# Kernel tuning notes

Hardware: AMD Instinct MI355X
Metric: run time of the kernel (lower is better)

The kernel has to match this reference:

```python
import jax, jax.numpy as jnp
import numpy as np

B, L1, L2, DIM_HID = 32, 64, 64, 256
FEAT = 2 * DIM_HID  # per-sequence feature dim; pair dim = 4*dim_hid


def setup_inputs() -> dict:
    key = jax.random.key(0)
    k1, k2, k3, k4, k5, k6 = jax.random.split(key, 6)
    x1 = jax.random.normal(k1, (B, L1, FEAT), dtype=jnp.float32)
    x2 = jax.random.normal(k2, (B, L2, FEAT), dtype=jnp.float32)
    # lengths in [1, L]; force max length so torch's dynamic max_len == L1*L2
    seq_lens1 = jax.random.randint(k3, (B,), 1, L1 + 1).at[0].set(L1)
    seq_lens2 = jax.random.randint(k4, (B,), 1, L2 + 1).at[0].set(L2)
    W = jax.random.normal(k5, (DIM_HID, 4 * DIM_HID), dtype=jnp.float32) * (1.0 / np.sqrt(4 * DIM_HID))
    b = jax.random.normal(k6, (DIM_HID,), dtype=jnp.float32) * 0.01
    return {"x1": x1, "seq_lens1": seq_lens1, "x2": x2, "seq_lens2": seq_lens2, "W": W, "b": b}


def reference(x1, seq_lens1, x2, seq_lens2, W, b):
    # Faithful to torch: for each sample, all (i,j) pairs with i<sl1, j<sl2 get
    # feature concat(x1[i], x2[j]); remaining rows (up to max_len = L1*L2) are
    # zero-padded BEFORE Linear+ReLU, so they contribute relu(b) to the sum.
    # Linear on concat == split GEMM: x1 @ W[:, :F].T + x2 @ W[:, F:].T + b,
    # which avoids materializing the [B, L1*L2, 4h] pair tensor.
    y1 = jnp.einsum('bif,hf->bih', x1, W[:, :FEAT])  # [B, L1, H]
    y2 = jnp.einsum('bjf,hf->bjh', x2, W[:, FEAT:])  # [B, L2, H]
    mask = (jnp.arange(L1)[None, :] < seq_lens1[:, None])[:, :, None] & \
           (jnp.arange(L2)[None, :] < seq_lens2[:, None])[:, None, :]  # [B, L1, L2]
    z = jnp.where(mask[..., None], y1[:, :, None, :] + y2[:, None, :, :] + b, b)
    y = jax.nn.relu(z)  # [B, L1, L2, H]; dropout is identity (eval / p handled)
    denom = (seq_lens1 * seq_lens2).astype(x1.dtype)[:, None]
    return y.sum(axis=(1, 2)) / denom
```

## Files before the change

kernel.cpp:

```cpp
#include <hip/hip_runtime.h>

#define BB 32
#define LL 64
#define HH 256
#define FF 512
#define WSTRIDE 1024
#define HT 16
#define BK 64
#define NKT (FF / BK)
#define YSTR 17

#define A1OFF 0
#define A2OFF 16384
#define W1OFF 32768
#define W2OFF 36864
#define BUFB  40960

typedef float float4v __attribute__((ext_vector_type(4)));
typedef short short8  __attribute__((ext_vector_type(8)));

static __device__ __forceinline__ unsigned int cvt_pk_bf16(float lo, float hi) {
    unsigned int r;
    asm("v_cvt_pk_bf16_f32 %0, %1, %2" : "=v"(r) : "v"(lo), "v"(hi));
    return r;
}

static __device__ __forceinline__ short8 cvt8(float4 lo, float4 hi) {
    union { short8 s; unsigned int u[4]; } o;
    o.u[0] = cvt_pk_bf16(lo.x, lo.y);
    o.u[1] = cvt_pk_bf16(lo.z, lo.w);
    o.u[2] = cvt_pk_bf16(hi.x, hi.y);
    o.u[3] = cvt_pk_bf16(hi.z, hi.w);
    return o.s;
}

static __device__ __forceinline__ void gl16(const float* g, void* l) {
    __builtin_amdgcn_global_load_lds(
        (const __attribute__((address_space(1))) void*)(const void*)g,
        (__attribute__((address_space(3))) void*)l, 16, 0, 0);
}

__global__ __launch_bounds__(256)
void fused_kernel(const float* __restrict__ x1,
                  const float* __restrict__ x2,
                  const float* __restrict__ W,
                  const int* __restrict__ s1p,
                  const int* __restrict__ s2p,
                  const float* __restrict__ bias,
                  float* __restrict__ out) {
    const int b  = blockIdx.x;
    const int h0 = blockIdx.y * HT;

    __shared__ __align__(16) unsigned char smem[2 * BUFB];
    float (*y1t)[YSTR]     = (float (*)[YSTR])(smem);
    float (*y2t)[YSTR]     = (float (*)[YSTR])(smem + 4352);
    float (*partial)[YSTR] = (float (*)[YSTR])(smem + 8704);

    const int t      = threadIdx.x;
    const int lane   = t & 63;
    const int wid    = t >> 6;
    const int srcSel = wid >> 1;
    const int mrow   = (wid & 1) * 32;
    const int lm     = lane & 15;
    const int quad   = lane >> 4;

    const int srow = t >> 4;
    const int sg   = (t & 15) ^ (srow & 7);

    const float* a1g = x1 + (size_t)(b * LL + srow) * FF + sg * 4;
    const float* a2g = x2 + (size_t)(b * LL + srow) * FF + sg * 4;
    const float* w1g = W + (size_t)(h0 + srow) * WSTRIDE + sg * 4;
    const float* w2g = w1g + FF;

    float4v acc[2];
    acc[0] = (float4v){0.f, 0.f, 0.f, 0.f};
    acc[1] = (float4v){0.f, 0.f, 0.f, 0.f};

    const int m     = lm & 7;
    const int offLo = (((quad * 2)     ^ m) * 16);
    const int offHi = (((quad * 2 + 1) ^ m) * 16);
    const int aRowOff = (srcSel ? A2OFF : A1OFF) + (mrow + lm) * 256;
    const int bRowOff = (srcSel ? W2OFF : W1OFF) + lm * 256;

    auto issue = [&](int kt, int bsel) {
        unsigned char* Lb = smem + bsel * BUFB;
        const int ko = kt * BK;
        #pragma unroll
        for (int q = 0; q < 4; ++q) {
            gl16(a1g + ko + (size_t)q * (16 * FF), Lb + A1OFF + q * 4096 + wid * 1024);
            gl16(a2g + ko + (size_t)q * (16 * FF), Lb + A2OFF + q * 4096 + wid * 1024);
        }
        gl16(w1g + ko, Lb + W1OFF + wid * 1024);
        gl16(w2g + ko, Lb + W2OFF + wid * 1024);
    };

    issue(0, 0);
    __syncthreads();

    for (int kt = 0; kt < NKT; ++kt) {
        if (kt + 1 < NKT) issue(kt + 1, (kt + 1) & 1);

        const unsigned char* Lb  = smem + (kt & 1) * BUFB;
        const unsigned char* pA0 = Lb + aRowOff;
        const unsigned char* pA1 = pA0 + 16 * 256;
        const unsigned char* pB  = Lb + bRowOff;

        #pragma unroll
        for (int ks = 0; ks < 2; ++ks) {
            const int kb = ks * 128;
            const float4 a0lo = *(const float4*)(pA0 + kb + offLo);
            const float4 a0hi = *(const float4*)(pA0 + kb + offHi);
            const float4 a1lo = *(const float4*)(pA1 + kb + offLo);
            const float4 a1hi = *(const float4*)(pA1 + kb + offHi);
            const float4 blo  = *(const float4*)(pB  + kb + offLo);
            const float4 bhi  = *(const float4*)(pB  + kb + offHi);
            const short8 a0 = cvt8(a0lo, a0hi);
            const short8 a1 = cvt8(a1lo, a1hi);
            const short8 b0 = cvt8(blo, bhi);
            acc[0] = __builtin_amdgcn_mfma_f32_16x16x32_bf16(a0, b0, acc[0], 0, 0, 0);
            acc[1] = __builtin_amdgcn_mfma_f32_16x16x32_bf16(a1, b0, acc[1], 0, 0, 0);
        }
        __syncthreads();
    }

    {
        float (*yt)[YSTR] = srcSel ? y2t : y1t;
        const float bv = srcSel ? bias[h0 + lm] : 0.0f;
        #pragma unroll
        for (int im = 0; im < 2; ++im)
            #pragma unroll
            for (int j = 0; j < 4; ++j)
                yt[mrow + im * 16 + quad * 4 + j][lm] = acc[im][j] + bv;
    }
    __syncthreads();

    const int n1 = s1p[b];
    const int n2 = s2p[b];
    const int h  = t & 15;
    const int ic = t >> 4;

    float r1[4];
    #pragma unroll
    for (int ii = 0; ii < 4; ++ii) {
        const int i = ic * 4 + ii;
        r1[ii] = (i < n1) ? y1t[i][h] : -1e30f;
    }

    float ac[4] = {0.f, 0.f, 0.f, 0.f};
    int j = 0;
    for (; j + 4 <= n2; j += 4) {
        const float v0 = y2t[j][h];
        const float v1 = y2t[j + 1][h];
        const float v2 = y2t[j + 2][h];
        const float v3 = y2t[j + 3][h];
        #pragma unroll
        for (int ii = 0; ii < 4; ++ii) {
            ac[ii] += fmaxf(r1[ii] + v0, 0.f);
            ac[ii] += fmaxf(r1[ii] + v1, 0.f);
            ac[ii] += fmaxf(r1[ii] + v2, 0.f);
            ac[ii] += fmaxf(r1[ii] + v3, 0.f);
        }
    }
    for (; j < n2; ++j) {
        const float v0 = y2t[j][h];
        #pragma unroll
        for (int ii = 0; ii < 4; ++ii)
            ac[ii] += fmaxf(r1[ii] + v0, 0.f);
    }
    partial[ic][h] = (ac[0] + ac[1]) + (ac[2] + ac[3]);
    __syncthreads();

    if (t < HT) {
        float s = 0.f;
        #pragma unroll
        for (int ic2 = 0; ic2 < 16; ++ic2)
            s += partial[ic2][t];
        const float denom = (float)(n1 * n2);
        const float pad = (float)(LL * LL) - denom;
        out[b * HH + h0 + t] = (s + pad * fmaxf(bias[h0 + t], 0.f)) / denom;
    }
}

extern "C" void kernel_launch(void* const* d_in, const int* in_sizes, int n_in,
                              void* d_out, int out_size, void* d_ws, size_t ws_size,
                              hipStream_t stream) {
    const float* x1 = (const float*)d_in[0];
    const int*   s1 = (const int*)d_in[1];
    const float* x2 = (const float*)d_in[2];
    const int*   s2 = (const int*)d_in[3];
    const float* W  = (const float*)d_in[4];
    const float* b  = (const float*)d_in[5];
    float* out = (float*)d_out;
    (void)d_ws; (void)ws_size;

    fused_kernel<<<dim3(BB, HH / HT), 256, 0, stream>>>(x1, x2, W, s1, s2, b, out);
}
```

Measured before the change: 76.93 us.

## Load GEMM operands directly from global into registers, dropping LDS staging

Replaces the double-buffered global-to-LDS async staging pipeline with direct per-lane float4 global loads feeding the bf16 MFMA. LDS use drops to the small reduction tables, which removes the per-tile barriers and could raise occupancy. In exchange, global loads are no longer coalesced across the wave's rows, and the latency overlap now relies on loop unrolling rather than explicit prefetch.

```diff
diff --git a/kernel.cpp b/kernel.cpp
--- a/kernel.cpp
+++ b/kernel.cpp
@@ -6,15 +6,7 @@
 #define FF 512
 #define WSTRIDE 1024
 #define HT 16
-#define BK 64
-#define NKT (FF / BK)
 #define YSTR 17
-
-#define A1OFF 0
-#define A2OFF 16384
-#define W1OFF 32768
-#define W2OFF 36864
-#define BUFB  40960
 
 typedef float float4v __attribute__((ext_vector_type(4)));
 typedef short short8  __attribute__((ext_vector_type(8)));
@@ -34,12 +26,6 @@
     return o.s;
 }
 
-static __device__ __forceinline__ void gl16(const float* g, void* l) {
-    __builtin_amdgcn_global_load_lds(
-        (const __attribute__((address_space(1))) void*)(const void*)g,
-        (__attribute__((address_space(3))) void*)l, 16, 0, 0);
-}
-
 __global__ __launch_bounds__(256)
 void fused_kernel(const float* __restrict__ x1,
                   const float* __restrict__ x2,
@@ -51,10 +37,9 @@
     const int b  = blockIdx.x;
     const int h0 = blockIdx.y * HT;
 
-    __shared__ __align__(16) unsigned char smem[2 * BUFB];
-    float (*y1t)[YSTR]     = (float (*)[YSTR])(smem);
-    float (*y2t)[YSTR]     = (float (*)[YSTR])(smem + 4352);
-    float (*partial)[YSTR] = (float (*)[YSTR])(smem + 8704);
+    __shared__ float y1t[LL][YSTR];
+    __shared__ float y2t[LL][YSTR];
+    __shared__ float partial[16][YSTR];
 
     const int t      = threadIdx.x;
     const int lane   = t & 63;
@@ -64,63 +49,29 @@
     const int lm     = lane & 15;
     const int quad   = lane >> 4;
 
-    const int srow = t >> 4;
-    const int sg   = (t & 15) ^ (srow & 7);
-
-    const float* a1g = x1 + (size_t)(b * LL + srow) * FF + sg * 4;
-    const float* a2g = x2 + (size_t)(b * LL + srow) * FF + sg * 4;
-    const float* w1g = W + (size_t)(h0 + srow) * WSTRIDE + sg * 4;
-    const float* w2g = w1g + FF;
+    const float* Xsrc = srcSel ? x2 : x1;
+    const float* aRow0 = Xsrc + (size_t)(b * LL + mrow + lm) * FF + quad * 8;
+    const float* aRow1 = aRow0 + (size_t)16 * FF;
+    const float* bRow  = W + (size_t)(h0 + lm) * WSTRIDE + srcSel * FF + quad * 8;
 
     float4v acc[2];
     acc[0] = (float4v){0.f, 0.f, 0.f, 0.f};
     acc[1] = (float4v){0.f, 0.f, 0.f, 0.f};
 
-    const int m     = lm & 7;
-    const int offLo = (((quad * 2)     ^ m) * 16);
-    const int offHi = (((quad * 2 + 1) ^ m) * 16);
-    const int aRowOff = (srcSel ? A2OFF : A1OFF) + (mrow + lm) * 256;
-    const int bRowOff = (srcSel ? W2OFF : W1OFF) + lm * 256;
-
-    auto issue = [&](int kt, int bsel) {
-        unsigned char* Lb = smem + bsel * BUFB;
-        const int ko = kt * BK;
-        #pragma unroll
-        for (int q = 0; q < 4; ++q) {
-            gl16(a1g + ko + (size_t)q * (16 * FF), Lb + A1OFF + q * 4096 + wid * 1024);
-            gl16(a2g + ko + (size_t)q * (16 * FF), Lb + A2OFF + q * 4096 + wid * 1024);
-        }
-        gl16(w1g + ko, Lb + W1OFF + wid * 1024);
-        gl16(w2g + ko, Lb + W2OFF + wid * 1024);
-    };
-
-    issue(0, 0);
-    __syncthreads();
-
-    for (int kt = 0; kt < NKT; ++kt) {
-        if (kt + 1 < NKT) issue(kt + 1, (kt + 1) & 1);
-
-        const unsigned char* Lb  = smem + (kt & 1) * BUFB;
-        const unsigned char* pA0 = Lb + aRowOff;
-        const unsigned char* pA1 = pA0 + 16 * 256;
-        const unsigned char* pB  = Lb + bRowOff;
-
-        #pragma unroll
-        for (int ks = 0; ks < 2; ++ks) {
-            const int kb = ks * 128;
-            const float4 a0lo = *(const float4*)(pA0 + kb + offLo);
-            const float4 a0hi = *(const float4*)(pA0 + kb + offHi);
-            const float4 a1lo = *(const float4*)(pA1 + kb + offLo);
-            const float4 a1hi = *(const float4*)(pA1 + kb + offHi);
-            const float4 blo  = *(const float4*)(pB  + kb + offLo);
-            const float4 bhi  = *(const float4*)(pB  + kb + offHi);
-            const short8 a0 = cvt8(a0lo, a0hi);
-            const short8 a1 = cvt8(a1lo, a1hi);
-            const short8 b0 = cvt8(blo, bhi);
-            acc[0] = __builtin_amdgcn_mfma_f32_16x16x32_bf16(a0, b0, acc[0], 0, 0, 0);
-            acc[1] = __builtin_amdgcn_mfma_f32_16x16x32_bf16(a1, b0, acc[1], 0, 0, 0);
-        }
-        __syncthreads();
+    #pragma unroll 4
+    for (int kt = 0; kt < FF / 32; ++kt) {
+        const int k = kt * 32;
+        const float4 a0lo = *(const float4*)(aRow0 + k);
+        const float4 a0hi = *(const float4*)(aRow0 + k + 4);
+        const float4 a1lo = *(const float4*)(aRow1 + k);
+        const float4 a1hi = *(const float4*)(aRow1 + k + 4);
+        const float4 blo  = *(const float4*)(bRow + k);
+        const float4 bhi  = *(const float4*)(bRow + k + 4);
+        const short8 a0 = cvt8(a0lo, a0hi);
+        const short8 a1 = cvt8(a1lo, a1hi);
+        const short8 b0 = cvt8(blo, bhi);
+        acc[0] = __builtin_amdgcn_mfma_f32_16x16x32_bf16(a0, b0, acc[0], 0, 0, 0);
+        acc[1] = __builtin_amdgcn_mfma_f32_16x16x32_bf16(a1, b0, acc[1], 0, 0, 0);
     }
 
     {
```

Result: slower. 89.07 us (+15.8%).
